# Performance work log

Hardware: AMD Instinct MI355X
Metric: run time of the kernel (lower is better)

## Reference

```python
import jax, jax.numpy as jnp
import numpy as np

NUM_CLASSES = 80
STRIDES = (8, 16, 32)
FEAT_HW = ((80, 80), (40, 40), (20, 20))
B = 32
MAX_GT = 60


def setup_inputs() -> dict:
    key = jax.random.key(0)
    ks = jax.random.split(key, 6)
    feats = {}
    for i, (s, (h, w)) in enumerate(zip(STRIDES, FEAT_HW)):
        feats[f"feat{s}"] = jax.random.normal(ks[i], (B, 5 + NUM_CLASSES, h, w), jnp.float32)
    u = jax.random.uniform(ks[3], (B, MAX_GT, 4), jnp.float32)
    # cx,cy in [0,640), w,h in [8,128): realistic pixel-space gt boxes for a 640x640 image
    gt_boxes = jnp.concatenate([u[..., :2] * 640.0, u[..., 2:] * 120.0 + 8.0], -1)
    gt_classes = jax.random.randint(ks[4], (B, MAX_GT), 0, NUM_CLASSES)
    num_gts = jax.random.randint(ks[5], (B,), 1, MAX_GT + 1)
    return dict(feat8=feats["feat8"], feat16=feats["feat16"], feat32=feats["feat32"],
                gt_boxes=gt_boxes, gt_classes=gt_classes, num_gts=num_gts)


def _decode(feat, stride):
    # torch get_output_and_grid: xy=(raw+grid)*stride, wh=exp(raw)*stride
    b, c, h, w = feat.shape
    yv, xv = jnp.meshgrid(jnp.arange(h), jnp.arange(w), indexing="ij")
    gx = xv.reshape(-1).astype(feat.dtype)  # [H*W]
    gy = yv.reshape(-1).astype(feat.dtype)
    out = feat.reshape(b, c, h * w).transpose(0, 2, 1)  # [B,A,C]
    xy = (out[..., :2] + jnp.stack([gx, gy], -1)[None]) * stride
    wh = jnp.exp(out[..., 2:4]) * stride
    return jnp.concatenate([xy, wh, out[..., 4:]], -1), gx, gy


def _pair_iou(a, b):
    # a: [G,4] xywh, b: [A,4] xywh -> [G,A] IoU (bboxes_iou, xyxy=False)
    tl = jnp.maximum(a[:, None, :2] - a[:, None, 2:] * 0.5, b[None, :, :2] - b[None, :, 2:] * 0.5)
    br = jnp.minimum(a[:, None, :2] + a[:, None, 2:] * 0.5, b[None, :, :2] + b[None, :, 2:] * 0.5)
    en = jnp.all(tl < br, -1)
    inter = jnp.where(en, jnp.prod(br - tl, -1), 0.0)
    area_a = jnp.prod(a[:, 2:], -1)
    area_b = jnp.prod(b[:, 2:], -1)
    return inter / (area_a[:, None] + area_b[None, :] - inter + 1e-16)


def _bce_logits(x, t):
    return jnp.maximum(x, 0.0) - x * t + jnp.log1p(jnp.exp(-jnp.abs(x)))


def _iou_loss(pred, tgt):
    # IOUloss(loss_type='iou'): 1 - iou^2, per box
    tl = jnp.maximum(pred[..., :2] - pred[..., 2:] * 0.5, tgt[..., :2] - tgt[..., 2:] * 0.5)
    br = jnp.minimum(pred[..., :2] + pred[..., 2:] * 0.5, tgt[..., :2] + tgt[..., 2:] * 0.5)
    en = jnp.all(tl < br, -1)
    inter = jnp.where(en, jnp.prod(br - tl, -1), 0.0)
    union = jnp.prod(pred[..., 2:], -1) + jnp.prod(tgt[..., 2:], -1) - inter
    iou = inter / (union + 1e-16)
    return 1.0 - iou ** 2


def _assign(boxes, cls_lo, obj_lo, gtb, gtc, vmask, cx, cy, st):
    # SimOTA per image. boxes [A,4], cls_lo [A,C], obj_lo [A], gtb [G,4], gtc [G] int,
    # vmask [G] bool (gt padding), cx/cy/st [A] anchor centers & strides.
    G, A = gtb.shape[0], boxes.shape[0]
    iou = _pair_iou(gtb, boxes)  # [G,A]
    gx, gy = gtb[:, :1], gtb[:, 1:2]
    gw, gh = gtb[:, 2:3], gtb[:, 3:4]
    in_box = ((cx[None] > gx - 0.5 * gw) & (cx[None] < gx + 0.5 * gw) &
              (cy[None] > gy - 0.5 * gh) & (cy[None] < gy + 0.5 * gh))
    R = 2.5  # center sampling radius (in strides)
    in_ctr = ((cx[None] > gx - R * st[None]) & (cx[None] < gx + R * st[None]) &
              (cy[None] > gy - R * st[None]) & (cy[None] < gy + R * st[None]))
    fg = ((in_box | in_ctr) & vmask[:, None]).any(0)  # [A] candidate anchors
    in_both = (in_box & in_ctr).astype(boxes.dtype)
    # pairwise cls cost: BCE(sqrt(sig(cls)*sig(obj)), onehot(gt_cls)).sum(-1),
    # decomposed to avoid the [G,A,C] tensor: sum_c bce0 + (bce1-bce0)[gt_cls]
    p = jnp.clip(jnp.sqrt(jax.nn.sigmoid(cls_lo) * jax.nn.sigmoid(obj_lo)[:, None]), 1e-7, 1.0 - 1e-7)
    bce1 = -jnp.log(p)          # [A,C]
    bce0 = -jnp.log(1.0 - p)    # [A,C]
    cls_cost = bce0.sum(-1)[None, :] + (bce1 - bce0)[:, gtc].T  # [G,A]
    cost = (cls_cost + 3.0 * (-jnp.log(iou + 1e-8))
            + 100000.0 * (1.0 - in_both)
            + 1e9 * (~fg)[None, :].astype(boxes.dtype)
            + 1e9 * (~vmask)[:, None].astype(boxes.dtype))
    K = 10  # n_candidate_k
    topk_ious, _ = jax.lax.top_k(iou * fg[None, :], K)
    dyn_k = jnp.maximum(topk_ious.sum(-1).astype(jnp.int32), 1)  # clamp(int(sum), min=1)
    _, pos = jax.lax.top_k(-cost, K)  # [G,K] lowest-cost anchors per gt
    sel = (jnp.arange(K)[None, :] < dyn_k[:, None]).astype(boxes.dtype)
    matching = jnp.zeros((G, A), boxes.dtype).at[jnp.arange(G)[:, None], pos].set(sel)
    matching = matching * vmask[:, None].astype(boxes.dtype)
    # resolve anchors claimed by >1 gt: keep min-cost gt
    conflict = matching.sum(0) > 1
    best_gt = jnp.argmin(cost, axis=0)  # [A]
    matching = jnp.where(conflict[None, :], jax.nn.one_hot(best_gt, G, dtype=matching.dtype).T, matching)
    fg_final = matching.sum(0) > 0  # [A]
    matched = jnp.argmax(matching, axis=0)  # [A]
    pred_iou = (matching * iou).sum(0)  # [A]
    cls_t = jax.nn.one_hot(gtc[matched], NUM_CLASSES, dtype=boxes.dtype) * pred_iou[:, None]
    reg_t = gtb[matched]
    return fg_final, cls_t, reg_t


def _forward(feat8, feat16, feat32, gt_boxes, gt_classes, num_gts):
    outs, cxs, cys, sts = [], [], [], []
    for f, s in zip((feat8, feat16, feat32), STRIDES):
        o, gx, gy = _decode(f, float(s))
        outs.append(o)
        cxs.append((gx + 0.5) * s)
        cys.append((gy + 0.5) * s)
        sts.append(jnp.full_like(gx, s))
    preds = jnp.concatenate(outs, 1)  # [B,A,5+C]
    cx = jnp.concatenate(cxs)
    cy = jnp.concatenate(cys)
    st = jnp.concatenate(sts)
    boxes = preds[..., :4]
    obj_lo = preds[..., 4]
    cls_lo = preds[..., 5:]
    vmask = jnp.arange(MAX_GT)[None, :] < num_gts[:, None]
    fg, cls_t, reg_t = jax.vmap(_assign, in_axes=(0, 0, 0, 0, 0, 0, None, None, None))(
        boxes, cls_lo, obj_lo, gt_boxes, gt_classes, vmask, cx, cy, st)
    # SimOTA assignment is no_grad in YOLOX: targets are constants wrt preds
    fg = jax.lax.stop_gradient(fg)
    cls_t = jax.lax.stop_gradient(cls_t)
    reg_t = jax.lax.stop_gradient(reg_t)
    fg_f = fg.astype(boxes.dtype)
    num_fg = jnp.maximum(fg_f.sum(), 1.0)
    loss_iou = (_iou_loss(boxes, reg_t) * fg_f).sum()
    loss_obj = _bce_logits(obj_lo, fg_f * 0.9).sum()  # obj_targets * 0.9 smoothing
    loss_cls = (_bce_logits(cls_lo, cls_t) * fg_f[..., None]).sum()
    REG_WEIGHT = 5.0
    return (REG_WEIGHT * loss_iou + loss_obj + loss_cls) / num_fg


def reference(feat8, feat16, feat32, gt_boxes, gt_classes, num_gts):
    return _forward(feat8, feat16, feat32, gt_boxes, gt_classes, num_gts)
```

## Files before the change

kernel.cpp:

```cpp
#include <hip/hip_runtime.h>

constexpr int kB = 32;
constexpr int kA = 8400;
constexpr int kG = 60;
constexpr int kC = 80;
constexpr int kK = 10;
constexpr int kNBx = (kA + 255)/256;
constexpr int kNB = kNBx * kB;

__device__ __forceinline__ float fexp(float x){ return __expf(x); }
__device__ __forceinline__ float flog(float x){ return __logf(x); }
__device__ __forceinline__ float frcp(float x){ return __builtin_amdgcn_rcpf(x); }
__device__ __forceinline__ float frsq(float x){ return __builtin_amdgcn_rsqf(x); }
__device__ __forceinline__ float fsqrt(float x){ return __builtin_amdgcn_sqrtf(x); }
__device__ __forceinline__ float fdiv(float a, float b){ return a * __builtin_amdgcn_rcpf(b); }
__device__ __forceinline__ float sigm(float x){ return frcp(1.0f + fexp(-x)); }
__device__ __forceinline__ float bce(float x, float t){
  return fmaxf(x, 0.0f) - x*t + flog(1.0f + fexp(-fabsf(x)));
}

__device__ __forceinline__ unsigned ordbits(float v){
  unsigned u = __float_as_uint(v);
  return (u & 0x80000000u) ? ~u : (u | 0x80000000u);
}
__device__ __forceinline__ float unpackf(unsigned k){
  return __uint_as_float((k & 0x80000000u) ? (k & 0x7fffffffu) : ~k);
}

struct AInfo { int x, y; float st; };
__device__ __forceinline__ AInfo ainfo(int a){
  AInfo r;
  if (a < 6400)      { r.x = a % 80;           r.y = a / 80;           r.st = 8.0f;  }
  else if (a < 8000) { int l = a-6400; r.x = l % 40; r.y = l / 40;     r.st = 16.0f; }
  else               { int l = a-8000; r.x = l % 20; r.y = l / 20;     r.st = 32.0f; }
  return r;
}

__device__ __forceinline__ float featv(const float* __restrict__ f8,
                                       const float* __restrict__ f16,
                                       const float* __restrict__ f32x,
                                       int b, int ch, int a){
  if (a < 6400) return f8 [(b*85 + ch)*6400 + a];
  if (a < 8000) return f16[(b*85 + ch)*1600 + (a - 6400)];
  return             f32x[(b*85 + ch)*400  + (a - 8000)];
}

__device__ __forceinline__ float pair_iou(float4 g, float4 p){
  float tlx = fmaxf(g.x - g.z*0.5f, p.x - p.z*0.5f);
  float tly = fmaxf(g.y - g.w*0.5f, p.y - p.w*0.5f);
  float brx = fminf(g.x + g.z*0.5f, p.x + p.z*0.5f);
  float bry = fminf(g.y + g.w*0.5f, p.y + p.w*0.5f);
  float inter = (tlx < brx && tly < bry) ? (brx-tlx)*(bry-tly) : 0.0f;
  return fdiv(inter, g.z*g.w + p.z*p.w - inter + 1e-16f);
}

__device__ __forceinline__ float cost_core(float iou, float cl, float obs, float b0sum,
                                           int a, float4 gt, int fg_a){
  AInfo ai = ainfo(a);
  float cx = ((float)ai.x + 0.5f)*ai.st;
  float cy = ((float)ai.y + 0.5f)*ai.st;
  bool in_box = (cx > gt.x - 0.5f*gt.z) && (cx < gt.x + 0.5f*gt.z)
             && (cy > gt.y - 0.5f*gt.w) && (cy < gt.y + 0.5f*gt.w);
  bool in_ctr = (cx > gt.x - 2.5f*ai.st) && (cx < gt.x + 2.5f*ai.st)
             && (cy > gt.y - 2.5f*ai.st) && (cy < gt.y + 2.5f*ai.st);
  float p = fsqrt(sigm(cl) * obs);
  p = fminf(fmaxf(p, 1e-7f), 1.0f - 1e-7f);
  float diff = -flog(p) + flog(1.0f - p);
  float c = b0sum + diff;
  c += 3.0f * (-flog(iou + 1e-8f));
  c += (in_box && in_ctr) ? 0.0f : 100000.0f;
  c += fg_a ? 0.0f : 1000000000.0f;
  return c;
}

__device__ __forceinline__ unsigned long long wave_max64(unsigned long long v){
  #pragma unroll
  for (int off = 32; off; off >>= 1){
    unsigned long long o = __shfl_xor(v, off, 64);
    if (o > v) v = o;
  }
  return v;
}

__global__ __launch_bounds__(256) void k_decode(
    const float* __restrict__ f8, const float* __restrict__ f16, const float* __restrict__ f32x,
    const float* __restrict__ gtb, const int* __restrict__ ngts,
    float* __restrict__ boxes, float* __restrict__ objl, float* __restrict__ b0s,
    float* __restrict__ bceS, float* __restrict__ obsA,
    int* __restrict__ fg, int* __restrict__ cnt, int* __restrict__ mtch){
  int b = blockIdx.y;
  int tid = threadIdx.x;
  int a = blockIdx.x*256 + tid;
  __shared__ float4 sg[kG];
  if (tid < kG) sg[tid] = ((const float4*)gtb)[b*kG + tid];
  __syncthreads();
  if (a >= kA) return;
  int ng = ngts[b];
  const float* base; int hw, off; float st_; int gx, gy;
  if (a < 6400)      { base=f8;   hw=6400; off=a;        st_=8.0f;  gx=off%80; gy=off/80; }
  else if (a < 8000) { base=f16;  hw=1600; off=a-6400;   st_=16.0f; gx=off%40; gy=off/40; }
  else               { base=f32x; hw=400;  off=a-8000;   st_=32.0f; gx=off%20; gy=off/20; }
  const float* p0 = base + ((size_t)b*85)*hw + off;
  float t0 = p0[0];
  float t1 = p0[(size_t)hw];
  float t2 = p0[(size_t)2*hw];
  float t3 = p0[(size_t)3*hw];
  float ob = p0[(size_t)4*hw];
  float4 bx;
  bx.x = (t0 + (float)gx) * st_;
  bx.y = (t1 + (float)gy) * st_;
  bx.z = fexp(t2) * st_;
  bx.w = fexp(t3) * st_;
  int idx = b*kA + a;
  ((float4*)boxes)[idx] = bx;
  objl[idx] = ob;
  float obs = sigm(ob);
  obsA[idx] = obs;
  float so = fsqrt(obs);
  float s = 0.0f;
  float sumCl = 0.0f;
  float slogv = 0.0f;
  const float* pc = p0 + (size_t)5*hw;
  #pragma unroll 2
  for (int grp = 0; grp < kC/8; ++grp){
    float prodS = 1.0f, prodV = 1.0f;
    #pragma unroll
    for (int j = 0; j < 8; ++j){
      float cl = pc[(size_t)(grp*8 + j)*hw];
      float u = fexp(-cl);
      float v = 1.0f + u;
      float p = so * frsq(v);
      p = fminf(fmaxf(p, 1e-7f), 1.0f - 1e-7f);
      prodS *= (1.0f - p);
      prodV *= v;
      sumCl += cl;
    }
    s -= flog(prodS);
    slogv += flog(prodV);
  }
  b0s[idx] = s;
  bceS[idx] = sumCl + slogv;
  float cx = ((float)gx + 0.5f)*st_;
  float cy = ((float)gy + 0.5f)*st_;
  int f = 0;
  for (int g = 0; g < ng; ++g){
    float4 gt = sg[g];
    bool in_box = (cx > gt.x - 0.5f*gt.z) && (cx < gt.x + 0.5f*gt.z)
               && (cy > gt.y - 0.5f*gt.w) && (cy < gt.y + 0.5f*gt.w);
    bool in_ctr = (cx > gt.x - 2.5f*st_) && (cx < gt.x + 2.5f*st_)
               && (cy > gt.y - 2.5f*st_) && (cy < gt.y + 2.5f*st_);
    if (in_box || in_ctr){ f = 1; break; }
  }
  fg[idx] = f;
  cnt[idx] = 0;
  mtch[idx] = 0x7fffffff;
}

__global__ __launch_bounds__(1024) void k_compact(
    const int* __restrict__ fg, unsigned short* __restrict__ alist, int* __restrict__ mcnt){
  int b = blockIdx.x;
  int tid = threadIdx.x;
  const int CH = 9;
  int start = tid*CH;
  int myf[CH]; int cl = 0;
  #pragma unroll
  for (int j = 0; j < CH; ++j){
    int a = start + j;
    int f = (a < kA) ? fg[b*kA + a] : 0;
    myf[j] = f; cl += f;
  }
  __shared__ int s1[1024], s2[1024];
  int* cur = s1; int* nxt = s2;
  cur[tid] = cl; __syncthreads();
  for (int off = 1; off < 1024; off <<= 1){
    int v = cur[tid];
    if (tid >= off) v += cur[tid - off];
    nxt[tid] = v; __syncthreads();
    int* t = cur; cur = nxt; nxt = t;
  }
  int o = cur[tid] - cl;
  unsigned short* out = alist + (size_t)b*kA;
  #pragma unroll
  for (int j = 0; j < CH; ++j){
    int a = start + j;
    if (a < kA && myf[j]) out[o++] = (unsigned short)a;
  }
  if (tid == 1023) mcnt[b] = cur[tid];
}

__global__ __launch_bounds__(256) void k_assign(
    const float* __restrict__ f8, const float* __restrict__ f16, const float* __restrict__ f32x,
    const float* __restrict__ gtb, const int* __restrict__ gtc, const int* __restrict__ ngts,
    const float* __restrict__ boxes, const float* __restrict__ obsA, const float* __restrict__ b0s,
    const int* __restrict__ fg, const unsigned short* __restrict__ alist, const int* __restrict__ mcnt,
    int* __restrict__ cnt, int* __restrict__ mtch){
  int b = blockIdx.x / kG;
  int g = blockIdx.x % kG;
  if (g >= ngts[b]) return;
  int tid = threadIdx.x;
  int lane = tid & 63, wid = tid >> 6;
  float4 gt = ((const float4*)gtb)[b*kG + g];
  int cls = gtc[b*kG + g];
  const float4* bx4 = (const float4*)boxes;
  const float* c8  = f8   + ((size_t)b*85 + 5 + cls)*6400;
  const float* c16 = f16  + ((size_t)b*85 + 5 + cls)*1600;
  const float* c32 = f32x + ((size_t)b*85 + 5 + cls)*400;
  int m = mcnt[b];
  bool full = (m < kK);
  int len = full ? kA : m;
  const unsigned short* al = alist + (size_t)b*kA;

  __shared__ unsigned long long lds_k[4*kK];
  __shared__ int lds_cnt[4];
  __shared__ int s_dynk;

  unsigned long long k1[kK];
  #pragma unroll
  for (int i = 0; i < kK; ++i) k1[i] = 0ull;

  for (int i = tid; i < len; i += 256){
    int a = full ? i : (int)al[i];
    int idx = b*kA + a;
    float4 bx = bx4[idx];
    float iou = pair_iou(gt, bx);
    int fga = full ? fg[idx] : 1;
    float v = fga ? iou : 0.0f;
    unsigned long long key1 = ((unsigned long long)ordbits(v) << 32) | (unsigned)(~a);
    if (key1 > k1[kK-1]){
      k1[kK-1] = key1;
      #pragma unroll
      for (int i2 = kK-1; i2 > 0; --i2)
        if (k1[i2] > k1[i2-1]){ unsigned long long t = k1[i2]; k1[i2] = k1[i2-1]; k1[i2-1] = t; }
    }
  }
  {
    unsigned long long wtop = 0ull;
    #pragma unroll
    for (int k = 0; k < kK; ++k){
      unsigned long long best = wave_max64(k1[0]);
      if (k1[0] == best){
        #pragma unroll
        for (int i2 = 0; i2 < kK-1; ++i2) k1[i2] = k1[i2+1];
        k1[kK-1] = 0ull;
      }
      if (lane == k) wtop = best;
    }
    if (lane < kK) lds_k[wid*kK + lane] = wtop;
  }
  __syncthreads();
  if (wid == 0){
    unsigned long long key = (lane < 4*kK) ? lds_k[lane] : 0ull;
    float ksum = 0.0f;
    #pragma unroll
    for (int k = 0; k < kK; ++k){
      unsigned long long best = wave_max64(key);
      if (key == best) key = 0ull;
      if (best) ksum += unpackf((unsigned)(best >> 32));
    }
    if (lane == 0) s_dynk = max((int)ksum, 1);
  }
  __syncthreads();
  int dynk = s_dynk;

  int x00,y00,nx0,n0, x01,y01,nx1,n1, x02,y02,nx2,n2;
  {
    auto rect = [&](float st, int W, int& rx0, int& ry0, int& rnx, int& rn){
      float lox = fmaxf(gt.x - 0.5f*gt.z, gt.x - 2.5f*st);
      float hix = fminf(gt.x + 0.5f*gt.z, gt.x + 2.5f*st);
      float loy = fmaxf(gt.y - 0.5f*gt.w, gt.y - 2.5f*st);
      float hiy = fminf(gt.y + 0.5f*gt.w, gt.y + 2.5f*st);
      float rs = frcp(st);
      int ax0 = max(0,   (int)floorf(lox*rs - 0.5f) - 1);
      int ax1 = min(W-1, (int)ceilf (hix*rs - 0.5f) + 1);
      int ay0 = max(0,   (int)floorf(loy*rs - 0.5f) - 1);
      int ay1 = min(W-1, (int)ceilf (hiy*rs - 0.5f) + 1);
      rx0 = ax0; ry0 = ay0;
      rnx = max(0, ax1 - ax0 + 1);
      int rny = max(0, ay1 - ay0 + 1);
      rn = rnx * rny;
    };
    rect( 8.0f, 80, x00, y00, nx0, n0);
    rect(16.0f, 40, x01, y01, nx1, n1);
    rect(32.0f, 20, x02, y02, nx2, n2);
  }
  int total = n0 + n1 + n2;

  unsigned long long ck = 0ull;
  int nvalid = 0;
  if (tid < total){
    int i = tid, ix, iy, a; float st;
    if (i < n0)           { ix = x00 + i % nx0; iy = y00 + i / nx0; a = iy*80 + ix;          st = 8.0f;  }
    else if (i < n0 + n1) { int j = i - n0;      ix = x01 + j % nx1; iy = y01 + j / nx1; a = 6400 + iy*40 + ix; st = 16.0f; }
    else                  { int j = i - n0 - n1; ix = x02 + j % nx2; iy = y02 + j / nx2; a = 8000 + iy*20 + ix; st = 32.0f; }
    float cx = ((float)ix + 0.5f)*st;
    float cy = ((float)iy + 0.5f)*st;
    bool in_box = (cx > gt.x - 0.5f*gt.z) && (cx < gt.x + 0.5f*gt.z)
               && (cy > gt.y - 0.5f*gt.w) && (cy < gt.y + 0.5f*gt.w);
    bool in_ctr = (cx > gt.x - 2.5f*st) && (cx < gt.x + 2.5f*st)
               && (cy > gt.y - 2.5f*st) && (cy < gt.y + 2.5f*st);
    if (in_box && in_ctr){
      int idx = b*kA + a;
      float4 bx = bx4[idx];
      float iou = pair_iou(gt, bx);
      float cl = (a < 6400) ? c8[a] : (a < 8000) ? c16[a-6400] : c32[a-8000];
      float c = cost_core(iou, cl, obsA[idx], b0s[idx], a, gt, 1);
      ck = ~(((unsigned long long)ordbits(c) << 32) | (unsigned)a);
      nvalid = 1;
    }
  }
  {
    unsigned long long bal = __ballot(nvalid);
    if (lane == 0) lds_cnt[wid] = __popcll(bal);
    unsigned long long wtop = 0ull;
    #pragma unroll
    for (int k = 0; k < kK; ++k){
      unsigned long long best = wave_max64(ck);
      if (ck == best) ck = 0ull;
      if (lane == k) wtop = best;
    }
    if (lane < kK) lds_k[wid*kK + lane] = wtop;
  }
  __syncthreads();
  int cnt_total = lds_cnt[0] + lds_cnt[1] + lds_cnt[2] + lds_cnt[3];
  bool fb = full || (dynk > cnt_total);

  if (!fb){
    if (wid == 0){
      unsigned long long key = (lane < 4*kK) ? lds_k[lane] : 0ull;
      unsigned long long mine = 0ull;
      #pragma unroll
      for (int k = 0; k < kK; ++k){
        unsigned long long best = wave_max64(key);
        if (key == best) key = 0ull;
        if (lane == k) mine = best;
      }
      if (lane < dynk && mine){
        int a = (int)((unsigned)(~mine));
        atomicAdd(&cnt[b*kA + a], 1);
        atomicMin(&mtch[b*kA + a], g);
      }
    }
    return;
  }

  __syncthreads();
  unsigned long long k2[kK];
  #pragma unroll
  for (int i = 0; i < kK; ++i) k2[i] = 0ull;
  for (int i = tid; i < len; i += 256){
    int a = full ? i : (int)al[i];
    int idx = b*kA + a;
    float4 bx = bx4[idx];
    float iou = pair_iou(gt, bx);
    int fga = full ? fg[idx] : 1;
    float cl = (a < 6400) ? c8[a] : (a < 8000) ? c16[a-6400] : c32[a-8000];
    float c = cost_core(iou, cl, obsA[idx], b0s[idx], a, gt, fga);
    unsigned long long key2 = ~(((unsigned long long)ordbits(c) << 32) | (unsigned)a);
    if (key2 > k2[kK-1]){
      k2[kK-1] = key2;
      #pragma unroll
      for (int i2 = kK-1; i2 > 0; --i2)
        if (k2[i2] > k2[i2-1]){ unsigned long long t = k2[i2]; k2[i2] = k2[i2-1]; k2[i2-1] = t; }
    }
  }
  {
    unsigned long long wtop = 0ull;
    #pragma unroll
    for (int k = 0; k < kK; ++k){
      unsigned long long best = wave_max64(k2[0]);
      if (k2[0] == best){
        #pragma unroll
        for (int i2 = 0; i2 < kK-1; ++i2) k2[i2] = k2[i2+1];
        k2[kK-1] = 0ull;
      }
      if (lane == k) wtop = best;
    }
    if (lane < kK) lds_k[wid*kK + lane] = wtop;
  }
  __syncthreads();
  if (wid == 0){
    unsigned long long key = (lane < 4*kK) ? lds_k[lane] : 0ull;
    unsigned long long mine = 0ull;
    #pragma unroll
    for (int k = 0; k < kK; ++k){
      unsigned long long best = wave_max64(key);
      if (key == best) key = 0ull;
      if (lane == k) mine = best;
    }
    if (lane < dynk && mine){
      int a = (int)((unsigned)(~mine));
      atomicAdd(&cnt[b*kA + a], 1);
      atomicMin(&mtch[b*kA + a], g);
    }
  }
}

__global__ __launch_bounds__(256) void k_loss(
    const float* __restrict__ f8, const float* __restrict__ f16, const float* __restrict__ f32x,
    const float* __restrict__ gtb, const int* __restrict__ gtc, const int* __restrict__ ngts,
    const float* __restrict__ boxes, const float* __restrict__ objl, const float* __restrict__ b0s,
    const float* __restrict__ bceS, const float* __restrict__ obsA,
    const int* __restrict__ fg, const int* __restrict__ cnt, const int* __restrict__ mtch,
    float4* __restrict__ pacc){
  int b = blockIdx.y;
  int a = blockIdx.x*256 + threadIdx.x;
  int tid = threadIdx.x;
  __shared__ float4 sg[kG];
  __shared__ int scls[kG];
  if (tid < kG){ sg[tid] = ((const float4*)gtb)[b*kG + tid]; scls[tid] = gtc[b*kG + tid]; }
  __syncthreads();
  float li = 0.0f, lo = 0.0f, lc = 0.0f, nf = 0.0f;
  bool valid = (a < kA);
  int idx = valid ? (b*kA + a) : (b*kA);
  int c = valid ? cnt[idx] : 0;
  float ob = valid ? objl[idx] : 0.0f;
  float4 bx = valid ? ((const float4*)boxes)[idx] : make_float4(0,0,1,1);

  float fgf = 0.0f; int mg = 0;
  if (valid && c == 1){ mg = mtch[idx]; fgf = 1.0f; }
  bool need = valid && (c > 1);
  if (__any(need)){
    if (need){
      int ng = ngts[b];
      float b0 = b0s[idx];
      float obs = obsA[idx];
      int fga = fg[idx];
      float bestc = 3.0e38f; int bg = 0;
      for (int g = 0; g < ng; ++g){
        float iou = pair_iou(sg[g], bx);
        float cl = featv(f8,f16,f32x,b,5+scls[g],a);
        float cst = cost_core(iou, cl, obs, b0, a, sg[g], fga);
        if (cst < bestc){ bestc = cst; bg = g; }
      }
      mg = bg; fgf = 1.0f;
    }
  }
  if (valid){
    lo = bce(ob, fgf*0.9f);
    if (fgf > 0.0f){
      nf = 1.0f;
      float4 r = sg[mg];
      float piou = pair_iou(r, bx);
      float tlx = fmaxf(bx.x - bx.z*0.5f, r.x - r.z*0.5f);
      float tly = fmaxf(bx.y - bx.w*0.5f, r.y - r.w*0.5f);
      float brx = fminf(bx.x + bx.z*0.5f, r.x + r.z*0.5f);
      float bry = fminf(bx.y + bx.w*0.5f, r.y + r.w*0.5f);
      float inter = (tlx < brx && tly < bry) ? (brx-tlx)*(bry-tly) : 0.0f;
      float un = bx.z*bx.w + r.z*r.w - inter;
      float iou = fdiv(inter, un + 1e-16f);
      li = 1.0f - iou*iou;
      int tc = scls[mg];
      float cl_tc = featv(f8,f16,f32x,b,5+tc,a);
      lc = bceS[idx] - piou * cl_tc;
    }
  }
  for (int off = 32; off > 0; off >>= 1){
    li += __shfl_down(li, off, 64);
    lo += __shfl_down(lo, off, 64);
    lc += __shfl_down(lc, off, 64);
    nf += __shfl_down(nf, off, 64);
  }
  __shared__ float4 wred[4];
  int wid = tid >> 6;
  if ((tid & 63) == 0) wred[wid] = make_float4(li, lo, lc, nf);
  __syncthreads();
  if (tid == 0){
    float4 t = wred[0];
    for (int w = 1; w < 4; ++w){
      float4 o = wred[w];
      t.x += o.x; t.y += o.y; t.z += o.z; t.w += o.w;
    }
    pacc[blockIdx.y * gridDim.x + blockIdx.x] = t;
  }
}

__global__ __launch_bounds__(256) void k_final(
    const float4* __restrict__ pacc, float* __restrict__ out){
  int tid = threadIdx.x;
  float li = 0.0f, lo = 0.0f, lc = 0.0f, nf = 0.0f;
  for (int i = tid; i < kNB; i += 256){
    float4 p = pacc[i];
    li += p.x; lo += p.y; lc += p.z; nf += p.w;
  }
  for (int off = 32; off > 0; off >>= 1){
    li += __shfl_down(li, off, 64);
    lo += __shfl_down(lo, off, 64);
    lc += __shfl_down(lc, off, 64);
    nf += __shfl_down(nf, off, 64);
  }
  __shared__ float4 wred[4];
  int wid = tid >> 6;
  if ((tid & 63) == 0) wred[wid] = make_float4(li, lo, lc, nf);
  __syncthreads();
  if (tid == 0){
    float4 t = wred[0];
    for (int w = 1; w < 4; ++w){
      float4 o = wred[w];
      t.x += o.x; t.y += o.y; t.z += o.z; t.w += o.w;
    }
    out[0] = (5.0f*t.x + t.y + t.z) * frcp(fmaxf(t.w, 1.0f));
  }
}

extern "C" void kernel_launch(void* const* d_in, const int* in_sizes, int n_in,
                              void* d_out, int out_size, void* d_ws, size_t ws_size,
                              hipStream_t stream) {
  (void)in_sizes; (void)n_in; (void)out_size; (void)ws_size;
  const float* f8   = (const float*)d_in[0];
  const float* f16  = (const float*)d_in[1];
  const float* f32x = (const float*)d_in[2];
  const float* gtb  = (const float*)d_in[3];
  const int*   gtc  = (const int*)d_in[4];
  const int*   ngts = (const int*)d_in[5];
  float* out = (float*)d_out;

  const size_t BA = (size_t)kB*kA;
  float* ws    = (float*)d_ws;
  float* boxes = ws;
  float* objl  = boxes + BA*4;
  float* b0s   = objl  + BA;
  float* bceS  = b0s   + BA;
  float* obsA  = bceS  + BA;
  int*   fg    = (int*)(obsA + BA);
  int*   cnt   = fg  + BA;
  int*   mtch  = cnt + BA;
  unsigned short* alist = (unsigned short*)(mtch + BA);
  int*   mcnt  = (int*)(alist + BA);
  float4* pacc = (float4*)(mcnt + kB);

  dim3 gBA(kNBx, kB);
  k_decode<<<gBA, dim3(256), 0, stream>>>(f8,f16,f32x,gtb,ngts,boxes,objl,b0s,bceS,obsA,fg,cnt,mtch);
  k_compact<<<dim3(kB), dim3(1024), 0, stream>>>(fg, alist, mcnt);
  k_assign<<<dim3(kB*kG), dim3(256), 0, stream>>>(f8,f16,f32x,gtb,gtc,ngts,boxes,obsA,b0s,fg,alist,mcnt,cnt,mtch);
  k_loss<<<gBA, dim3(256), 0, stream>>>(f8,f16,f32x,gtb,gtc,ngts,boxes,objl,b0s,bceS,obsA,fg,cnt,mtch,pacc);
  k_final<<<dim3(1), dim3(256), 0, stream>>>(pacc, out);
}
```

Measured before the change: 207.8 us.

## Fuse foreground compaction into decode via ballot+atomic and process two anchors per thread

Removes the separate k_compact kernel by building the per-image foreground anchor list inside k_decode using wave ballots, a block-level sum and an atomicAdd on a per-image counter zeroed by a memset. Each decode thread now handles two adjacent anchors with float2 loads to widen memory accesses. This saves a kernel launch and a reread of the fg array. In exchange, the compacted list is no longer in ascending anchor order, which could affect downstream tie-breaking if assignment depends on order.

```diff
diff --git a/kernel.cpp b/kernel.cpp
--- a/kernel.cpp
+++ b/kernel.cpp
@@ -7,6 +7,7 @@
 constexpr int kK = 10;
 constexpr int kNBx = (kA + 255)/256;
 constexpr int kNB = kNBx * kB;
+constexpr int kNPx = (kA/2 + 255)/256;
 
 __device__ __forceinline__ float fexp(float x){ return __expf(x); }
 __device__ __forceinline__ float flog(float x){ return __logf(x); }
@@ -87,105 +88,113 @@
     const float* __restrict__ gtb, const int* __restrict__ ngts,
     float* __restrict__ boxes, float* __restrict__ objl, float* __restrict__ b0s,
     float* __restrict__ bceS, float* __restrict__ obsA,
-    int* __restrict__ fg, int* __restrict__ cnt, int* __restrict__ mtch){
+    int* __restrict__ fg, int* __restrict__ cnt, int* __restrict__ mtch,
+    unsigned short* __restrict__ alist, int* __restrict__ mcnt){
   int b = blockIdx.y;
   int tid = threadIdx.x;
-  int a = blockIdx.x*256 + tid;
+  int lane = tid & 63, wid = tid >> 6;
+  int p = blockIdx.x*256 + tid;
   __shared__ float4 sg[kG];
+  __shared__ int swb[4];
+  __shared__ int sbase;
   if (tid < kG) sg[tid] = ((const float4*)gtb)[b*kG + tid];
   __syncthreads();
-  if (a >= kA) return;
+  bool alive = (p < kA/2);
+  int a = alive ? p*2 : 0;
   int ng = ngts[b];
-  const float* base; int hw, off; float st_; int gx, gy;
-  if (a < 6400)      { base=f8;   hw=6400; off=a;        st_=8.0f;  gx=off%80; gy=off/80; }
-  else if (a < 8000) { base=f16;  hw=1600; off=a-6400;   st_=16.0f; gx=off%40; gy=off/40; }
-  else               { base=f32x; hw=400;  off=a-8000;   st_=32.0f; gx=off%20; gy=off/20; }
+  const float* base; int hw, off; float st_; int W;
+  if (a < 6400)      { base=f8;   hw=6400; off=a;        st_=8.0f;  W=80; }
+  else if (a < 8000) { base=f16;  hw=1600; off=a-6400;   st_=16.0f; W=40; }
+  else               { base=f32x; hw=400;  off=a-8000;   st_=32.0f; W=20; }
+  int gx0 = off % W, gy0 = off / W;
+  int gx1 = gx0 + 1, gy1 = gy0;
+  if (gx1 == W){ gx1 = 0; gy1++; }
   const float* p0 = base + ((size_t)b*85)*hw + off;
-  float t0 = p0[0];
-  float t1 = p0[(size_t)hw];
-  float t2 = p0[(size_t)2*hw];
-  float t3 = p0[(size_t)3*hw];
-  float ob = p0[(size_t)4*hw];
-  float4 bx;
-  bx.x = (t0 + (float)gx) * st_;
-  bx.y = (t1 + (float)gy) * st_;
-  bx.z = fexp(t2) * st_;
-  bx.w = fexp(t3) * st_;
+  float2 t0 = *(const float2*)(p0);
+  float2 t1 = *(const float2*)(p0 + (size_t)hw);
+  float2 t2 = *(const float2*)(p0 + 2*(size_t)hw);
+  float2 t3 = *(const float2*)(p0 + 3*(size_t)hw);
+  float2 ob = *(const float2*)(p0 + 4*(size_t)hw);
+  float4 bx0, bx1;
+  bx0.x = (t0.x + (float)gx0) * st_;  bx0.y = (t1.x + (float)gy0) * st_;
+  bx0.z = fexp(t2.x) * st_;           bx0.w = fexp(t3.x) * st_;
+  bx1.x = (t0.y + (float)gx1) * st_;  bx1.y = (t1.y + (float)gy1) * st_;
+  bx1.z = fexp(t2.y) * st_;           bx1.w = fexp(t3.y) * st_;
   int idx = b*kA + a;
-  ((float4*)boxes)[idx] = bx;
-  objl[idx] = ob;
-  float obs = sigm(ob);
-  obsA[idx] = obs;
-  float so = fsqrt(obs);
-  float s = 0.0f;
-  float sumCl = 0.0f;
-  float slogv = 0.0f;
-  const float* pc = p0 + (size_t)5*hw;
+  float obs0 = sigm(ob.x), obs1 = sigm(ob.y);
+  float so0 = fsqrt(obs0), so1 = fsqrt(obs1);
+  float s0 = 0.0f, s1 = 0.0f;
+  float sc0 = 0.0f, sc1 = 0.0f;
+  float sv0 = 0.0f, sv1 = 0.0f;
+  const float* pc = p0 + 5*(size_t)hw;
   #pragma unroll 2
   for (int grp = 0; grp < kC/8; ++grp){
-    float prodS = 1.0f, prodV = 1.0f;
+    float pS0 = 1.0f, pS1 = 1.0f, pV0 = 1.0f, pV1 = 1.0f;
     #pragma unroll
     for (int j = 0; j < 8; ++j){
-      float cl = pc[(size_t)(grp*8 + j)*hw];
-      float u = fexp(-cl);
-      float v = 1.0f + u;
-      float p = so * frsq(v);
-      p = fminf(fmaxf(p, 1e-7f), 1.0f - 1e-7f);
-      prodS *= (1.0f - p);
-      prodV *= v;
-      sumCl += cl;
-    }
-    s -= flog(prodS);
-    slogv += flog(prodV);
-  }
-  b0s[idx] = s;
-  bceS[idx] = sumCl + slogv;
-  float cx = ((float)gx + 0.5f)*st_;
-  float cy = ((float)gy + 0.5f)*st_;
-  int f = 0;
-  for (int g = 0; g < ng; ++g){
-    float4 gt = sg[g];
-    bool in_box = (cx > gt.x - 0.5f*gt.z) && (cx < gt.x + 0.5f*gt.z)
-               && (cy > gt.y - 0.5f*gt.w) && (cy < gt.y + 0.5f*gt.w);
-    bool in_ctr = (cx > gt.x - 2.5f*st_) && (cx < gt.x + 2.5f*st_)
-               && (cy > gt.y - 2.5f*st_) && (cy < gt.y + 2.5f*st_);
-    if (in_box || in_ctr){ f = 1; break; }
-  }
-  fg[idx] = f;
-  cnt[idx] = 0;
-  mtch[idx] = 0x7fffffff;
-}
-
-__global__ __launch_bounds__(1024) void k_compact(
-    const int* __restrict__ fg, unsigned short* __restrict__ alist, int* __restrict__ mcnt){
-  int b = blockIdx.x;
-  int tid = threadIdx.x;
-  const int CH = 9;
-  int start = tid*CH;
-  int myf[CH]; int cl = 0;
-  #pragma unroll
-  for (int j = 0; j < CH; ++j){
-    int a = start + j;
-    int f = (a < kA) ? fg[b*kA + a] : 0;
-    myf[j] = f; cl += f;
-  }
-  __shared__ int s1[1024], s2[1024];
-  int* cur = s1; int* nxt = s2;
-  cur[tid] = cl; __syncthreads();
-  for (int off = 1; off < 1024; off <<= 1){
-    int v = cur[tid];
-    if (tid >= off) v += cur[tid - off];
-    nxt[tid] = v; __syncthreads();
-    int* t = cur; cur = nxt; nxt = t;
-  }
-  int o = cur[tid] - cl;
+      float2 cl = *(const float2*)(pc + (size_t)(grp*8 + j)*hw);
+      {
+        float u = fexp(-cl.x); float v = 1.0f + u;
+        float pp = so0 * frsq(v);
+        pp = fminf(fmaxf(pp, 1e-7f), 1.0f - 1e-7f);
+        pS0 *= (1.0f - pp); pV0 *= v; sc0 += cl.x;
+      }
+      {
+        float u = fexp(-cl.y); float v = 1.0f + u;
+        float pp = so1 * frsq(v);
+        pp = fminf(fmaxf(pp, 1e-7f), 1.0f - 1e-7f);
+        pS1 *= (1.0f - pp); pV1 *= v; sc1 += cl.y;
+      }
+    }
+    s0 -= flog(pS0); s1 -= flog(pS1);
+    sv0 += flog(pV0); sv1 += flog(pV1);
+  }
+  float cx0 = ((float)gx0 + 0.5f)*st_, cy0 = ((float)gy0 + 0.5f)*st_;
+  float cx1 = ((float)gx1 + 0.5f)*st_, cy1 = ((float)gy1 + 0.5f)*st_;
+  int f0 = 0, f1 = 0;
+  if (alive){
+    for (int g = 0; g < ng; ++g){
+      float4 gt = sg[g];
+      bool ib0 = (cx0 > gt.x - 0.5f*gt.z) && (cx0 < gt.x + 0.5f*gt.z)
+              && (cy0 > gt.y - 0.5f*gt.w) && (cy0 < gt.y + 0.5f*gt.w);
+      bool ic0 = (cx0 > gt.x - 2.5f*st_) && (cx0 < gt.x + 2.5f*st_)
+              && (cy0 > gt.y - 2.5f*st_) && (cy0 < gt.y + 2.5f*st_);
+      if (ib0 | ic0) f0 = 1;
+      bool ib1 = (cx1 > gt.x - 0.5f*gt.z) && (cx1 < gt.x + 0.5f*gt.z)
+              && (cy1 > gt.y - 0.5f*gt.w) && (cy1 < gt.y + 0.5f*gt.w);
+      bool ic1 = (cx1 > gt.x - 2.5f*st_) && (cx1 < gt.x + 2.5f*st_)
+              && (cy1 > gt.y - 2.5f*st_) && (cy1 < gt.y + 2.5f*st_);
+      if (ib1 | ic1) f1 = 1;
+      if (f0 & f1) break;
+    }
+  }
+  if (alive){
+    ((float4*)boxes)[idx]   = bx0;
+    ((float4*)boxes)[idx+1] = bx1;
+    objl[idx]   = ob.x;  objl[idx+1]   = ob.y;
+    obsA[idx]   = obs0;  obsA[idx+1]   = obs1;
+    b0s[idx]    = s0;    b0s[idx+1]    = s1;
+    bceS[idx]   = sc0 + sv0; bceS[idx+1] = sc1 + sv1;
+    fg[idx]     = f0;    fg[idx+1]     = f1;
+    cnt[idx]    = 0;     cnt[idx+1]    = 0;
+    mtch[idx]   = 0x7fffffff; mtch[idx+1] = 0x7fffffff;
+  }
+  unsigned long long m0 = __ballot(f0);
+  unsigned long long m1 = __ballot(f1);
+  int wtot = __popcll(m0) + __popcll(m1);
+  if (lane == 0) swb[wid] = wtot;
+  __syncthreads();
+  if (tid == 0){
+    int t = swb[0] + swb[1] + swb[2] + swb[3];
+    sbase = (t > 0) ? atomicAdd(mcnt + b, t) : 0;
+  }
+  __syncthreads();
+  int wbase = sbase;
+  for (int w = 0; w < wid; ++w) wbase += swb[w];
+  unsigned long long lt = ((unsigned long long)1 << lane) - 1ull;
   unsigned short* out = alist + (size_t)b*kA;
-  #pragma unroll
-  for (int j = 0; j < CH; ++j){
-    int a = start + j;
-    if (a < kA && myf[j]) out[o++] = (unsigned short)a;
-  }
-  if (tid == 1023) mcnt[b] = cur[tid];
+  if (f0) out[wbase + __popcll(m0 & lt)] = (unsigned short)a;
+  if (f1) out[wbase + __popcll(m0) + __popcll(m1 & lt)] = (unsigned short)(a+1);
 }
 
 __global__ __launch_bounds__(256) void k_assign(
@@ -528,10 +537,11 @@
   int*   mcnt  = (int*)(alist + BA);
   float4* pacc = (float4*)(mcnt + kB);
 
+  hipMemsetAsync(mcnt, 0, kB*sizeof(int), stream);
+  dim3 gD(kNPx, kB);
+  k_decode<<<gD, dim3(256), 0, stream>>>(f8,f16,f32x,gtb,ngts,boxes,objl,b0s,bceS,obsA,fg,cnt,mtch,alist,mcnt);
+  k_assign<<<dim3(kB*kG), dim3(256), 0, stream>>>(f8,f16,f32x,gtb,gtc,ngts,boxes,obsA,b0s,fg,alist,mcnt,cnt,mtch);
   dim3 gBA(kNBx, kB);
-  k_decode<<<gBA, dim3(256), 0, stream>>>(f8,f16,f32x,gtb,ngts,boxes,objl,b0s,bceS,obsA,fg,cnt,mtch);
-  k_compact<<<dim3(kB), dim3(1024), 0, stream>>>(fg, alist, mcnt);
-  k_assign<<<dim3(kB*kG), dim3(256), 0, stream>>>(f8,f16,f32x,gtb,gtc,ngts,boxes,obsA,b0s,fg,alist,mcnt,cnt,mtch);
   k_loss<<<gBA, dim3(256), 0, stream>>>(f8,f16,f32x,gtb,gtc,ngts,boxes,objl,b0s,bceS,obsA,fg,cnt,mtch,pacc);
   k_final<<<dim3(1), dim3(256), 0, stream>>>(pacc, out);
 }
```

New measurement: 233.1 us. 12.2% more time.

## Replace fg-anchor compaction with zero-masked boxes and prefetch class logits

Applied to the files above, without the earlier changes.

Removes the per-image compaction kernel and instead has the decode kernel write a copy of the boxes zeroed for non-candidate anchors, so the assignment kernel scans all anchors with coalesced loads rather than a gathered compacted list. The decode class loop also prefetches the next group of eight class logits into registers. This saves a launch and indirect loads, but every (image, gt) block now scans the full anchor set, and extra box storage is written.

```diff
diff --git a/kernel.cpp b/kernel.cpp
--- a/kernel.cpp
+++ b/kernel.cpp
@@ -85,7 +85,8 @@
 __global__ __launch_bounds__(256) void k_decode(
     const float* __restrict__ f8, const float* __restrict__ f16, const float* __restrict__ f32x,
     const float* __restrict__ gtb, const int* __restrict__ ngts,
-    float* __restrict__ boxes, float* __restrict__ objl, float* __restrict__ b0s,
+    float* __restrict__ boxes, float* __restrict__ boxesZ,
+    float* __restrict__ objl, float* __restrict__ b0s,
     float* __restrict__ bceS, float* __restrict__ obsA,
     int* __restrict__ fg, int* __restrict__ cnt, int* __restrict__ mtch){
   int b = blockIdx.y;
@@ -101,11 +102,15 @@
   else if (a < 8000) { base=f16;  hw=1600; off=a-6400;   st_=16.0f; gx=off%40; gy=off/40; }
   else               { base=f32x; hw=400;  off=a-8000;   st_=32.0f; gx=off%20; gy=off/20; }
   const float* p0 = base + ((size_t)b*85)*hw + off;
+  const float* pc = p0 + (size_t)5*hw;
   float t0 = p0[0];
   float t1 = p0[(size_t)hw];
   float t2 = p0[(size_t)2*hw];
   float t3 = p0[(size_t)3*hw];
   float ob = p0[(size_t)4*hw];
+  float cur[8];
+  #pragma unroll
+  for (int j = 0; j < 8; ++j) cur[j] = pc[(size_t)j*hw];
   float4 bx;
   bx.x = (t0 + (float)gx) * st_;
   bx.y = (t1 + (float)gy) * st_;
@@ -120,13 +125,17 @@
   float s = 0.0f;
   float sumCl = 0.0f;
   float slogv = 0.0f;
-  const float* pc = p0 + (size_t)5*hw;
-  #pragma unroll 2
+  #pragma unroll 1
   for (int grp = 0; grp < kC/8; ++grp){
+    float nxt[8];
+    if (grp < kC/8 - 1){
+      #pragma unroll
+      for (int j = 0; j < 8; ++j) nxt[j] = pc[(size_t)((grp+1)*8 + j)*hw];
+    }
     float prodS = 1.0f, prodV = 1.0f;
     #pragma unroll
     for (int j = 0; j < 8; ++j){
-      float cl = pc[(size_t)(grp*8 + j)*hw];
+      float cl = cur[j];
       float u = fexp(-cl);
       float v = 1.0f + u;
       float p = so * frsq(v);
@@ -137,6 +146,8 @@
     }
     s -= flog(prodS);
     slogv += flog(prodV);
+    #pragma unroll
+    for (int j = 0; j < 8; ++j) cur[j] = nxt[j];
   }
   b0s[idx] = s;
   bceS[idx] = sumCl + slogv;
@@ -152,47 +163,17 @@
     if (in_box || in_ctr){ f = 1; break; }
   }
   fg[idx] = f;
+  ((float4*)boxesZ)[idx] = f ? bx : make_float4(0.0f,0.0f,0.0f,0.0f);
   cnt[idx] = 0;
   mtch[idx] = 0x7fffffff;
-}
-
-__global__ __launch_bounds__(1024) void k_compact(
-    const int* __restrict__ fg, unsigned short* __restrict__ alist, int* __restrict__ mcnt){
-  int b = blockIdx.x;
-  int tid = threadIdx.x;
-  const int CH = 9;
-  int start = tid*CH;
-  int myf[CH]; int cl = 0;
-  #pragma unroll
-  for (int j = 0; j < CH; ++j){
-    int a = start + j;
-    int f = (a < kA) ? fg[b*kA + a] : 0;
-    myf[j] = f; cl += f;
-  }
-  __shared__ int s1[1024], s2[1024];
-  int* cur = s1; int* nxt = s2;
-  cur[tid] = cl; __syncthreads();
-  for (int off = 1; off < 1024; off <<= 1){
-    int v = cur[tid];
-    if (tid >= off) v += cur[tid - off];
-    nxt[tid] = v; __syncthreads();
-    int* t = cur; cur = nxt; nxt = t;
-  }
-  int o = cur[tid] - cl;
-  unsigned short* out = alist + (size_t)b*kA;
-  #pragma unroll
-  for (int j = 0; j < CH; ++j){
-    int a = start + j;
-    if (a < kA && myf[j]) out[o++] = (unsigned short)a;
-  }
-  if (tid == 1023) mcnt[b] = cur[tid];
 }
 
 __global__ __launch_bounds__(256) void k_assign(
     const float* __restrict__ f8, const float* __restrict__ f16, const float* __restrict__ f32x,
     const float* __restrict__ gtb, const int* __restrict__ gtc, const int* __restrict__ ngts,
-    const float* __restrict__ boxes, const float* __restrict__ obsA, const float* __restrict__ b0s,
-    const int* __restrict__ fg, const unsigned short* __restrict__ alist, const int* __restrict__ mcnt,
+    const float* __restrict__ boxes, const float* __restrict__ boxesZ,
+    const float* __restrict__ obsA, const float* __restrict__ b0s,
+    const int* __restrict__ fg,
     int* __restrict__ cnt, int* __restrict__ mtch){
   int b = blockIdx.x / kG;
   int g = blockIdx.x % kG;
@@ -202,13 +183,10 @@
   float4 gt = ((const float4*)gtb)[b*kG + g];
   int cls = gtc[b*kG + g];
   const float4* bx4 = (const float4*)boxes;
+  const float4* bz4 = (const float4*)boxesZ;
   const float* c8  = f8   + ((size_t)b*85 + 5 + cls)*6400;
   const float* c16 = f16  + ((size_t)b*85 + 5 + cls)*1600;
   const float* c32 = f32x + ((size_t)b*85 + 5 + cls)*400;
-  int m = mcnt[b];
-  bool full = (m < kK);
-  int len = full ? kA : m;
-  const unsigned short* al = alist + (size_t)b*kA;
 
   __shared__ unsigned long long lds_k[4*kK];
   __shared__ int lds_cnt[4];
@@ -218,14 +196,10 @@
   #pragma unroll
   for (int i = 0; i < kK; ++i) k1[i] = 0ull;
 
-  for (int i = tid; i < len; i += 256){
-    int a = full ? i : (int)al[i];
-    int idx = b*kA + a;
-    float4 bx = bx4[idx];
-    float iou = pair_iou(gt, bx);
-    int fga = full ? fg[idx] : 1;
-    float v = fga ? iou : 0.0f;
-    unsigned long long key1 = ((unsigned long long)ordbits(v) << 32) | (unsigned)(~a);
+  for (int i = tid; i < kA; i += 256){
+    float4 bx = bz4[b*kA + i];
+    float v = pair_iou(gt, bx);
+    unsigned long long key1 = ((unsigned long long)ordbits(v) << 32) | (unsigned)(~i);
     if (key1 > k1[kK-1]){
       k1[kK-1] = key1;
       #pragma unroll
@@ -322,7 +296,7 @@
   }
   __syncthreads();
   int cnt_total = lds_cnt[0] + lds_cnt[1] + lds_cnt[2] + lds_cnt[3];
-  bool fb = full || (dynk > cnt_total);
+  bool fb = (dynk > cnt_total);
 
   if (!fb){
     if (wid == 0){
@@ -347,15 +321,14 @@
   unsigned long long k2[kK];
   #pragma unroll
   for (int i = 0; i < kK; ++i) k2[i] = 0ull;
-  for (int i = tid; i < len; i += 256){
-    int a = full ? i : (int)al[i];
-    int idx = b*kA + a;
+  for (int i = tid; i < kA; i += 256){
+    int idx = b*kA + i;
     float4 bx = bx4[idx];
     float iou = pair_iou(gt, bx);
-    int fga = full ? fg[idx] : 1;
-    float cl = (a < 6400) ? c8[a] : (a < 8000) ? c16[a-6400] : c32[a-8000];
-    float c = cost_core(iou, cl, obsA[idx], b0s[idx], a, gt, fga);
-    unsigned long long key2 = ~(((unsigned long long)ordbits(c) << 32) | (unsigned)a);
+    int fga = fg[idx];
+    float cl = (i < 6400) ? c8[i] : (i < 8000) ? c16[i-6400] : c32[i-8000];
+    float c = cost_core(iou, cl, obsA[idx], b0s[idx], i, gt, fga);
+    unsigned long long key2 = ~(((unsigned long long)ordbits(c) << 32) | (unsigned)i);
     if (key2 > k2[kK-1]){
       k2[kK-1] = key2;
       #pragma unroll
@@ -515,23 +488,21 @@
   float* out = (float*)d_out;
 
   const size_t BA = (size_t)kB*kA;
-  float* ws    = (float*)d_ws;
-  float* boxes = ws;
-  float* objl  = boxes + BA*4;
-  float* b0s   = objl  + BA;
-  float* bceS  = b0s   + BA;
-  float* obsA  = bceS  + BA;
-  int*   fg    = (int*)(obsA + BA);
-  int*   cnt   = fg  + BA;
-  int*   mtch  = cnt + BA;
-  unsigned short* alist = (unsigned short*)(mtch + BA);
-  int*   mcnt  = (int*)(alist + BA);
-  float4* pacc = (float4*)(mcnt + kB);
+  float* ws     = (float*)d_ws;
+  float* boxes  = ws;
+  float* boxesZ = boxes  + BA*4;
+  float* objl   = boxesZ + BA*4;
+  float* b0s    = objl   + BA;
+  float* bceS   = b0s    + BA;
+  float* obsA   = bceS   + BA;
+  int*   fg     = (int*)(obsA + BA);
+  int*   cnt    = fg  + BA;
+  int*   mtch   = cnt + BA;
+  float4* pacc  = (float4*)(mtch + BA);
 
   dim3 gBA(kNBx, kB);
-  k_decode<<<gBA, dim3(256), 0, stream>>>(f8,f16,f32x,gtb,ngts,boxes,objl,b0s,bceS,obsA,fg,cnt,mtch);
-  k_compact<<<dim3(kB), dim3(1024), 0, stream>>>(fg, alist, mcnt);
-  k_assign<<<dim3(kB*kG), dim3(256), 0, stream>>>(f8,f16,f32x,gtb,gtc,ngts,boxes,obsA,b0s,fg,alist,mcnt,cnt,mtch);
+  k_decode<<<gBA, dim3(256), 0, stream>>>(f8,f16,f32x,gtb,ngts,boxes,boxesZ,objl,b0s,bceS,obsA,fg,cnt,mtch);
+  k_assign<<<dim3(kB*kG), dim3(256), 0, stream>>>(f8,f16,f32x,gtb,gtc,ngts,boxes,boxesZ,obsA,b0s,fg,cnt,mtch);
   k_loss<<<gBA, dim3(256), 0, stream>>>(f8,f16,f32x,gtb,gtc,ngts,boxes,objl,b0s,bceS,obsA,fg,cnt,mtch,pacc);
   k_final<<<dim3(1), dim3(256), 0, stream>>>(pacc, out);
 }
```

Result: faster. 203.4 us (-2.1%).
